# Kernel tuning notes

Hardware: AMD Instinct MI355X
Metric: run time of the kernel (lower is better)

Reference implementation:

```python
import jax, jax.numpy as jnp
import numpy as np

BATCH, T, D_MODEL, DIM = 8, 4096, 512, 512
R_MIN, R_MAX, MAX_PHASE = 0.0, 1.0, 6.28


def setup_inputs() -> dict:
    key = jax.random.key(0)
    ks = jax.random.split(key, 8)
    x = jax.random.normal(ks[0], (BATCH, T, D_MODEL), dtype=jnp.float32)
    h0 = jnp.zeros((BATCH, 1, DIM), dtype=jnp.float32)
    # nu_log / theta_log per the module's initializers
    u1 = jax.random.uniform(ks[1], (DIM,))
    nu_log = jnp.log(-0.5 * jnp.log(u1 * (R_MAX ** 2 - R_MIN ** 2) + R_MIN ** 2)).astype(jnp.float32)
    u2 = jax.random.uniform(ks[2], (DIM,))
    theta_log = jnp.log(MAX_PHASE * u2).astype(jnp.float32)
    # B ~ N(0,1)/sqrt(2*D_in), C ~ N(0,1)/sqrt(D_out)
    B_re = (jax.random.normal(ks[3], (D_MODEL, DIM)) / jnp.sqrt(2.0 * D_MODEL)).astype(jnp.float32)
    B_im = (jax.random.normal(ks[4], (D_MODEL, DIM)) / jnp.sqrt(2.0 * D_MODEL)).astype(jnp.float32)
    C_re = (jax.random.normal(ks[5], (DIM, D_MODEL)) / jnp.sqrt(float(D_MODEL))).astype(jnp.float32)
    C_im = (jax.random.normal(ks[6], (DIM, D_MODEL)) / jnp.sqrt(float(D_MODEL))).astype(jnp.float32)
    D_param = jax.random.normal(ks[7], (D_MODEL,)).astype(jnp.float32)
    # gamma_log = log(sqrt(1 - |Lambda|^2)) with Lambda from nu/theta
    diag_lambda = jnp.exp(-jnp.exp(nu_log) + 1j * jnp.exp(theta_log))
    gamma_log = jnp.log(jnp.sqrt(1.0 - jnp.abs(diag_lambda) ** 2)).astype(jnp.float32)
    return {"x": x, "h0": h0, "nu_log": nu_log, "theta_log": theta_log,
            "B_re": B_re, "B_im": B_im, "C_re": C_re, "C_im": C_im,
            "D_param": D_param, "gamma_log": gamma_log}


def _binary_op(ei, ej):
    a_i, b_i = ei
    a_j, b_j = ej
    return (a_j * a_i, a_j * b_i + b_j)


def reference(x, h0, nu_log, theta_log, B_re, B_im, C_re, C_im, D_param, gamma_log):
    B, T_len, _ = x.shape
    Lambda = jnp.exp(-jnp.exp(nu_log) + 1j * jnp.exp(theta_log))            # (N,) complex
    B_norm = (B_re + 1j * B_im) * jnp.exp(gamma_log)[None, :]               # (D,N) complex
    C = C_re + 1j * C_im                                                     # (N,D) complex
    # Input projection: Bu[b,t,n] = sum_d x[b,t,d] * B_norm[d,n]
    Bu = jnp.einsum('btd,dn->btn', x.astype(jnp.complex64), B_norm)
    Bu = jnp.concatenate([h0.astype(jnp.complex64), Bu], axis=1)             # (B,T+1,N)
    Lam = jnp.broadcast_to(Lambda, Bu.shape)                                 # (B,T+1,N)
    _, H = jax.lax.associative_scan(_binary_op, (Lam, Bu), axis=1)
    H = H[:, 1:]                                                             # (B,T,N)
    y = jnp.einsum('btn,nd->btd', H, C).real + D_param * x                   # (B,T,D)
    new_h = H[:, -1:]                                                        # (B,1,N) complex
    return (y, new_h)
```

## Files before the change

kernel.cpp:

```cpp
#include <hip/hip_runtime.h>

#define T_LEN 4096
#define DMODEL 512
#define DIM 512
#define NBATCH 8
#define MROWS (NBATCH * T_LEN)
#define NCHUNK 128
#define LCHUNK 32

typedef __attribute__((ext_vector_type(8))) short short8;
typedef __attribute__((ext_vector_type(4))) float float4v;

__device__ __forceinline__ ushort f2b(float f) {
    union { float fl; unsigned u; } v; v.fl = f;
    unsigned u = v.u;
    return (ushort)((u + 0x7FFFu + ((u >> 16) & 1u)) >> 16);
}
__device__ __forceinline__ float b2f(ushort u) {
    union { unsigned u; float f; } v; v.u = (unsigned)u << 16; return v.f;
}

__device__ __forceinline__ void glds16(const ushort* g, ushort* l) {
    __builtin_amdgcn_global_load_lds(
        (const __attribute__((address_space(1))) void*)g,
        (__attribute__((address_space(3))) void*)l, 16, 0, 0);
}

#define XBLK (MROWS * 512 / 4 / 256)
#define BBLK (1024 * 512 / 256)
#define CBLK (512 * 1024 / 256)

__global__ __launch_bounds__(256) void k_prep(const float* __restrict__ x,
                                              const float* __restrict__ B_re,
                                              const float* __restrict__ B_im,
                                              const float* __restrict__ gamma_log,
                                              const float* __restrict__ C_re,
                                              const float* __restrict__ C_im,
                                              ushort* __restrict__ Xb,
                                              ushort* __restrict__ BT,
                                              ushort* __restrict__ CT) {
    int bb = blockIdx.x;
    if (bb < XBLK) {
        int i = (bb * 256 + threadIdx.x) * 4;
        float4 v = *(const float4*)(x + i);
        ushort4 o;
        o.x = f2b(v.x); o.y = f2b(v.y); o.z = f2b(v.z); o.w = f2b(v.w);
        *(ushort4*)(Xb + i) = o;
    } else if (bb < XBLK + BBLK) {
        int idx = (bb - XBLK) * 256 + threadIdx.x;
        int n = idx >> 9;
        int d = idx & 511;
        float v;
        if (n < 512) v = B_re[d * 512 + n] * __expf(gamma_log[n]);
        else { int nn = n - 512; v = B_im[d * 512 + nn] * __expf(gamma_log[nn]); }
        BT[idx] = f2b(v);
    } else {
        int idx = (bb - XBLK - BBLK) * 256 + threadIdx.x;
        int d = idx >> 10;
        int k = idx & 1023;
        float v = (k < 512) ? C_re[k * 512 + d] : -C_im[(k - 512) * 512 + d];
        CT[idx] = f2b(v);
    }
}


template<int K>
__device__ __forceinline__ void stage_tile(const ushort* gA0, const ushort* gB0, int kt,
                                           ushort* sAb, ushort* sBb, int wave) {
#pragma unroll
    for (int c = 0; c < 4; c++) {
        glds16(gA0 + (size_t)(c * 8) * K + (size_t)kt * 64, &sAb[(wave * 32 + c * 8) * 64]);
        glds16(gB0 + (size_t)(c * 8) * K + (size_t)kt * 64, &sBb[(wave * 32 + c * 8) * 64]);
    }
}

__device__ __forceinline__ void compute_tile(const ushort* sAb, const ushort* sBb,
                                             int wm, int wn, int lr, int quad,
                                             float4v acc[4][4]) {
#pragma unroll
    for (int kk = 0; kk < 2; kk++) {
        short8 af[4], bfr[4];
#pragma unroll
        for (int i = 0; i < 4; i++) {
            int row = wm + i * 16 + lr;
            af[i] = *(const short8*)&sAb[row * 64 + (((kk * 4 + quad) ^ (row & 7)) * 8)];
        }
#pragma unroll
        for (int j = 0; j < 4; j++) {
            int row = wn + j * 16 + lr;
            bfr[j] = *(const short8*)&sBb[row * 64 + (((kk * 4 + quad) ^ (row & 7)) * 8)];
        }
#pragma unroll
        for (int i = 0; i < 4; i++)
#pragma unroll
            for (int j = 0; j < 4; j++)
                acc[i][j] = __builtin_amdgcn_mfma_f32_16x16x32_bf16(af[i], bfr[j], acc[i][j], 0, 0, 0);
    }
}

template<int K, int MODE, int NBN>
__global__ __launch_bounds__(256) void k_gemm(
    const ushort* __restrict__ A, const ushort* __restrict__ Bt,
    ushort* __restrict__ oRe, ushort* __restrict__ oIm,
    float* __restrict__ y, const float* __restrict__ x, const float* __restrict__ Dp) {
    __shared__ ushort sA[2][128 * 64];
    __shared__ ushort sB[2][128 * 64];
    const int tid = threadIdx.x;
    const int L = blockIdx.x;
    const int xcd = L & 7;
    const int slot = L >> 3;
    const int m0 = (xcd * 32 + slot / NBN) * 128;
    const int n0 = (slot % NBN) * 128;
    const int wave = tid >> 6;
    const int lane = tid & 63;
    const int wm = (wave >> 1) * 64;
    const int wn = (wave & 1) * 64;
    const int lr = lane & 15;
    const int quad = lane >> 4;

    const int srow = lane >> 3;
    const int schunk = (lane & 7) ^ srow;
    const ushort* gA0 = A + (size_t)(m0 + wave * 32 + srow) * K + schunk * 8;
    const ushort* gB0 = Bt + (size_t)(n0 + wave * 32 + srow) * K + schunk * 8;

    float4v acc[4][4];
#pragma unroll
    for (int i = 0; i < 4; i++)
#pragma unroll
        for (int j = 0; j < 4; j++) {
            float4v z = {0.f, 0.f, 0.f, 0.f};
            acc[i][j] = z;
        }

    const int NT = K / 64;

    stage_tile<K>(gA0, gB0, 0, &sA[0][0], &sB[0][0], wave);
    __syncthreads();

    for (int t = 0; t < NT; t += 2) {
        stage_tile<K>(gA0, gB0, t + 1, &sA[1][0], &sB[1][0], wave);
        compute_tile(&sA[0][0], &sB[0][0], wm, wn, lr, quad, acc);
        __syncthreads();

        if (t + 2 < NT)
            stage_tile<K>(gA0, gB0, t + 2, &sA[0][0], &sB[0][0], wave);
        compute_tile(&sA[1][0], &sB[1][0], wm, wn, lr, quad, acc);
        __syncthreads();
    }

#pragma unroll
    for (int i = 0; i < 4; i++) {
#pragma unroll
        for (int j = 0; j < 4; j++) {
            int gmb = m0 + wm + i * 16 + quad * 4;
            int gn = n0 + wn + j * 16 + lr;
#pragma unroll
            for (int r = 0; r < 4; r++) {
                float v = acc[i][j][r];
                int row = gmb + r;
                if (MODE == 1) {
                    if (gn < 512) oRe[(size_t)row * 512 + gn] = f2b(v);
                    else oIm[(size_t)row * 512 + (gn - 512)] = f2b(v);
                } else {
                    size_t o = (size_t)row * 512 + gn;
                    y[o] = v + Dp[gn] * x[o];
                }
            }
        }
    }
}


__device__ __forceinline__ void lambda_of(const float* nu_log, const float* theta_log,
                                          int n, float& lre, float& lim) {
    float e = __expf(nu_log[n]);
    float th = __expf(theta_log[n]);
    float rad = __expf(-e);
    float s, c;
    __sincosf(th, &s, &c);
    lre = rad * c;
    lim = rad * s;
}

__global__ __launch_bounds__(256) void k_scan1(const ushort* __restrict__ BuRe,
                                               const ushort* __restrict__ BuIm,
                                               const float* __restrict__ nu_log,
                                               const float* __restrict__ theta_log,
                                               float* __restrict__ cRe, float* __restrict__ cIm) {
    int n2 = threadIdx.x;
    int b = blockIdx.x >> 7;
    int c = blockIdx.x & 127;
    float lre0, lim0, lre1, lim1;
    lambda_of(nu_log, theta_log, 2 * n2, lre0, lim0);
    lambda_of(nu_log, theta_log, 2 * n2 + 1, lre1, lim1);
    float hr0 = 0.f, hi0 = 0.f, hr1 = 0.f, hi1 = 0.f;
    size_t base = ((size_t)b * T_LEN + (size_t)c * LCHUNK) * 512 + 2 * n2;
#pragma unroll 8
    for (int j = 0; j < LCHUNK; j++) {
        ushort2 ur = *(const ushort2*)(BuRe + base + (size_t)j * 512);
        ushort2 ui = *(const ushort2*)(BuIm + base + (size_t)j * 512);
        float br0 = b2f(ur.x), br1 = b2f(ur.y), bi0 = b2f(ui.x), bi1 = b2f(ui.y);
        float nr0 = lre0 * hr0 - lim0 * hi0 + br0;
        float ni0 = lre0 * hi0 + lim0 * hr0 + bi0;
        hr0 = nr0; hi0 = ni0;
        float nr1 = lre1 * hr1 - lim1 * hi1 + br1;
        float ni1 = lre1 * hi1 + lim1 * hr1 + bi1;
        hr1 = nr1; hi1 = ni1;
    }
    size_t co = ((size_t)b * NCHUNK + c) * 512 + 2 * n2;
    *(float2*)(cRe + co) = make_float2(hr0, hr1);
    *(float2*)(cIm + co) = make_float2(hi0, hi1);
}

__global__ __launch_bounds__(64) void k_scan2(const float* __restrict__ cRe,
                                              const float* __restrict__ cIm,
                                              const float* __restrict__ h0,
                                              const float* __restrict__ nu_log,
                                              const float* __restrict__ theta_log,
                                              float* __restrict__ pRe, float* __restrict__ pIm,
                                              float* __restrict__ newH, int newh_mode) {
    int idx = blockIdx.x * 64 + threadIdx.x;
    int b = idx >> 9;
    int n = idx & 511;
    float lre, lim;
    lambda_of(nu_log, theta_log, n, lre, lim);
    float Lr = lre, Li = lim;
#pragma unroll
    for (int s = 0; s < 5; s++) {
        float nr = Lr * Lr - Li * Li;
        float ni = 2.f * Lr * Li;
        Lr = nr; Li = ni;
    }
    float cr = h0[b * 512 + n];
    float ci = 0.f;
#pragma unroll 4
    for (int c = 0; c < NCHUNK; c++) {
        size_t o = ((size_t)b * NCHUNK + c) * 512 + n;
        pRe[o] = cr;
        pIm[o] = ci;
        float ar = cRe[o], ai = cIm[o];
        float nr = Lr * cr - Li * ci + ar;
        float ni = Lr * ci + Li * cr + ai;
        cr = nr; ci = ni;
    }
    size_t ci_idx = (size_t)b * 512 + n;
    if (newh_mode == 1) {
        newH[ci_idx] = cr;
        newH[(size_t)NBATCH * 512 + ci_idx] = ci;
    } else if (newh_mode == 2) {
        newH[ci_idx] = cr;
    } else {
        newH[ci_idx * 2] = cr;
        newH[ci_idx * 2 + 1] = ci;
    }
}

__global__ __launch_bounds__(256) void k_scan3(const ushort* __restrict__ BuRe,
                                               const ushort* __restrict__ BuIm,
                                               const float* __restrict__ pRe,
                                               const float* __restrict__ pIm,
                                               const float* __restrict__ nu_log,
                                               const float* __restrict__ theta_log,
                                               ushort* __restrict__ Hbf) {
    int n2 = threadIdx.x;
    int b = blockIdx.x >> 7;
    int c = blockIdx.x & 127;
    float lre0, lim0, lre1, lim1;
    lambda_of(nu_log, theta_log, 2 * n2, lre0, lim0);
    lambda_of(nu_log, theta_log, 2 * n2 + 1, lre1, lim1);
    size_t co = ((size_t)b * NCHUNK + c) * 512 + 2 * n2;
    float2 frv = *(const float2*)(pRe + co);
    float2 fiv = *(const float2*)(pIm + co);
    float fr0 = frv.x, fr1 = frv.y, fi0 = fiv.x, fi1 = fiv.y;
    float pr0 = lre0, pi0 = lim0, pr1 = lre1, pi1 = lim1;
    float hr0 = 0.f, hi0 = 0.f, hr1 = 0.f, hi1 = 0.f;
    size_t row0 = (size_t)b * T_LEN + (size_t)c * LCHUNK;
#pragma unroll 4
    for (int j = 0; j < LCHUNK; j++) {
        size_t base = (row0 + j) * 512 + 2 * n2;
        ushort2 ur = *(const ushort2*)(BuRe + base);
        ushort2 ui = *(const ushort2*)(BuIm + base);
        float br0 = b2f(ur.x), br1 = b2f(ur.y), bi0 = b2f(ui.x), bi1 = b2f(ui.y);
        float nr0 = lre0 * hr0 - lim0 * hi0 + br0;
        float ni0 = lre0 * hi0 + lim0 * hr0 + bi0;
        hr0 = nr0; hi0 = ni0;
        float nr1 = lre1 * hr1 - lim1 * hi1 + br1;
        float ni1 = lre1 * hi1 + lim1 * hr1 + bi1;
        hr1 = nr1; hi1 = ni1;
        float vr0 = hr0 + pr0 * fr0 - pi0 * fi0;
        float vi0 = hi0 + pr0 * fi0 + pi0 * fr0;
        float vr1 = hr1 + pr1 * fr1 - pi1 * fi1;
        float vi1 = hi1 + pr1 * fi1 + pi1 * fr1;
        size_t hrow = (row0 + j) * 1024;
        ushort2 wre, wim;
        wre.x = f2b(vr0); wre.y = f2b(vr1);
        wim.x = f2b(vi0); wim.y = f2b(vi1);
        *(ushort2*)(Hbf + hrow + 2 * n2) = wre;
        *(ushort2*)(Hbf + hrow + 512 + 2 * n2) = wim;
        float npr0 = pr0 * lre0 - pi0 * lim0;
        float npi0 = pr0 * lim0 + pi0 * lre0;
        pr0 = npr0; pi0 = npi0;
        float npr1 = pr1 * lre1 - pi1 * lim1;
        float npi1 = pr1 * lim1 + pi1 * lre1;
        pr1 = npr1; pi1 = npi1;
    }
}


extern "C" void kernel_launch(void* const* d_in, const int* in_sizes, int n_in,
                              void* d_out, int out_size, void* d_ws, size_t ws_size,
                              hipStream_t stream) {
    const float* x         = (const float*)d_in[0];
    const float* h0        = (const float*)d_in[1];
    const float* nu_log    = (const float*)d_in[2];
    const float* theta_log = (const float*)d_in[3];
    const float* B_re      = (const float*)d_in[4];
    const float* B_im      = (const float*)d_in[5];
    const float* C_re      = (const float*)d_in[6];
    const float* C_im      = (const float*)d_in[7];
    const float* D_param   = (const float*)d_in[8];
    const float* gamma_log = (const float*)d_in[9];

    char* ws = (char*)d_ws;
    size_t off = 0;
    ushort* Xb   = (ushort*)(ws + off); off += (size_t)MROWS * 512 * 2;
    ushort* BT   = (ushort*)(ws + off); off += (size_t)1024 * 512 * 2;
    ushort* CT   = (ushort*)(ws + off); off += (size_t)512 * 1024 * 2;
    ushort* BuRe = (ushort*)(ws + off); off += (size_t)MROWS * 512 * 2;
    ushort* BuIm = (ushort*)(ws + off); off += (size_t)MROWS * 512 * 2;
    ushort* Hbf  = (ushort*)(ws + off); off += (size_t)MROWS * 1024 * 2;
    float*  cRe  = (float*)(ws + off); off += (size_t)NBATCH * NCHUNK * 512 * 4;
    float*  cIm  = (float*)(ws + off); off += (size_t)NBATCH * NCHUNK * 512 * 4;
    float*  pRe  = (float*)(ws + off); off += (size_t)NBATCH * NCHUNK * 512 * 4;
    float*  pIm  = (float*)(ws + off); off += (size_t)NBATCH * NCHUNK * 512 * 4;

    float* y_out = (float*)d_out;
    float* newH  = (float*)d_out + (size_t)MROWS * 512;

    const int tail = out_size - MROWS * 512;
    int newh_mode = 0;
    if (tail == NBATCH * 512 * 2) newh_mode = 1;
    else if (tail == NBATCH * 512) newh_mode = 2;

    k_prep<<<dim3(XBLK + BBLK + CBLK), dim3(256), 0, stream>>>(
        x, B_re, B_im, gamma_log, C_re, C_im, Xb, BT, CT);

    k_gemm<512, 1, 8><<<dim3(2048), dim3(256), 0, stream>>>(
        Xb, BT, BuRe, BuIm, nullptr, nullptr, nullptr);

    k_scan1<<<dim3(NBATCH * NCHUNK), dim3(256), 0, stream>>>(BuRe, BuIm, nu_log, theta_log, cRe, cIm);
    k_scan2<<<dim3(NBATCH * 512 / 64), dim3(64), 0, stream>>>(cRe, cIm, h0, nu_log, theta_log, pRe, pIm, newH, newh_mode);
    k_scan3<<<dim3(NBATCH * NCHUNK), dim3(256), 0, stream>>>(BuRe, BuIm, pRe, pIm, nu_log, theta_log, Hbf);

    k_gemm<1024, 2, 4><<<dim3(1024), dim3(256), 0, stream>>>(
        Hbf, CT, nullptr, nullptr, y_out, x, D_param);
}
```

Before: 287.2 us.

## Enlarge GEMM tiles to 256x128 with 8 waves and triple-buffered LDS pipeline

Both bf16 MFMA GEMMs now use 256x128 block tiles with 512 threads instead of 128x128 with 256. The old double-buffered loop with __syncthreads is replaced by a triple-buffered ring: tiles are prefetched two steps ahead and each step waits with explicit vmcnt counts and raw s_barrier calls. MFMA sections are wrapped in s_setprio. The aim is to hide global-to-LDS load latency and improve operand reuse. In exchange, LDS use grows to about 144KB per block, which leaves one block per CU and halves the grid size. An unused helper that passes a null LDS pointer is also added.

```diff
diff --git a/kernel.cpp b/kernel.cpp
--- a/kernel.cpp
+++ b/kernel.cpp
@@ -64,14 +64,23 @@
 }
 
 
+__device__ __forceinline__ void stage_tileA(const ushort* gA0, long koff, ushort* sAb,
+                                            int wave) {
+#pragma unroll
+    for (int c = 0; c < 4; c++)
+        glds16(gA0 + (long)(c * 8) * 0 + koff + 0, nullptr);
+}
+
 template<int K>
 __device__ __forceinline__ void stage_tile(const ushort* gA0, const ushort* gB0, int kt,
                                            ushort* sAb, ushort* sBb, int wave) {
-#pragma unroll
-    for (int c = 0; c < 4; c++) {
-        glds16(gA0 + (size_t)(c * 8) * K + (size_t)kt * 64, &sAb[(wave * 32 + c * 8) * 64]);
-        glds16(gB0 + (size_t)(c * 8) * K + (size_t)kt * 64, &sBb[(wave * 32 + c * 8) * 64]);
-    }
+    const long ko = (long)kt * 64;
+#pragma unroll
+    for (int c = 0; c < 4; c++)
+        glds16(gA0 + (long)(c * 8) * K + ko, &sAb[(wave * 32 + c * 8) * 64]);
+#pragma unroll
+    for (int c = 0; c < 2; c++)
+        glds16(gB0 + (long)(c * 8) * K + ko, &sBb[(wave * 16 + c * 8) * 64]);
 }
 
 __device__ __forceinline__ void compute_tile(const ushort* sAb, const ushort* sBb,
@@ -90,26 +99,29 @@
             int row = wn + j * 16 + lr;
             bfr[j] = *(const short8*)&sBb[row * 64 + (((kk * 4 + quad) ^ (row & 7)) * 8)];
         }
+        __builtin_amdgcn_s_setprio(1);
 #pragma unroll
         for (int i = 0; i < 4; i++)
 #pragma unroll
             for (int j = 0; j < 4; j++)
                 acc[i][j] = __builtin_amdgcn_mfma_f32_16x16x32_bf16(af[i], bfr[j], acc[i][j], 0, 0, 0);
+        __builtin_amdgcn_s_setprio(0);
     }
 }
 
 template<int K, int MODE, int NBN>
-__global__ __launch_bounds__(256) void k_gemm(
+__global__ __launch_bounds__(512) void k_gemm(
     const ushort* __restrict__ A, const ushort* __restrict__ Bt,
     ushort* __restrict__ oRe, ushort* __restrict__ oIm,
     float* __restrict__ y, const float* __restrict__ x, const float* __restrict__ Dp) {
-    __shared__ ushort sA[2][128 * 64];
-    __shared__ ushort sB[2][128 * 64];
+    const int NT = K / 64;
+    __shared__ ushort sA[3][256 * 64];
+    __shared__ ushort sB[3][128 * 64];
     const int tid = threadIdx.x;
     const int L = blockIdx.x;
     const int xcd = L & 7;
     const int slot = L >> 3;
-    const int m0 = (xcd * 32 + slot / NBN) * 128;
+    const int m0 = (xcd * 16 + slot / NBN) * 256;
     const int n0 = (slot % NBN) * 128;
     const int wave = tid >> 6;
     const int lane = tid & 63;
@@ -121,7 +133,7 @@
     const int srow = lane >> 3;
     const int schunk = (lane & 7) ^ srow;
     const ushort* gA0 = A + (size_t)(m0 + wave * 32 + srow) * K + schunk * 8;
-    const ushort* gB0 = Bt + (size_t)(n0 + wave * 32 + srow) * K + schunk * 8;
+    const ushort* gB0 = Bt + (size_t)(n0 + wave * 16 + srow) * K + schunk * 8;
 
     float4v acc[4][4];
 #pragma unroll
@@ -132,20 +144,28 @@
             acc[i][j] = z;
         }
 
-    const int NT = K / 64;
-
-    stage_tile<K>(gA0, gB0, 0, &sA[0][0], &sB[0][0], wave);
-    __syncthreads();
-
-    for (int t = 0; t < NT; t += 2) {
-        stage_tile<K>(gA0, gB0, t + 1, &sA[1][0], &sB[1][0], wave);
-        compute_tile(&sA[0][0], &sB[0][0], wm, wn, lr, quad, acc);
-        __syncthreads();
-
+    ushort *a0 = &sA[0][0], *a1 = &sA[1][0], *a2 = &sA[2][0];
+    ushort *b0 = &sB[0][0], *b1 = &sB[1][0], *b2 = &sB[2][0];
+
+    stage_tile<K>(gA0, gB0, 0, a0, b0, wave);
+    stage_tile<K>(gA0, gB0, 1, a1, b1, wave);
+    asm volatile("s_waitcnt vmcnt(6)" ::: "memory");
+    __builtin_amdgcn_s_barrier();
+    __builtin_amdgcn_sched_barrier(0);
+
+    for (int t = 0; t < NT; ++t) {
         if (t + 2 < NT)
-            stage_tile<K>(gA0, gB0, t + 2, &sA[0][0], &sB[0][0], wave);
-        compute_tile(&sA[1][0], &sB[1][0], wm, wn, lr, quad, acc);
-        __syncthreads();
+            stage_tile<K>(gA0, gB0, t + 2, a2, b2, wave);
+        compute_tile(a0, b0, wm, wn, lr, quad, acc);
+        if (t + 2 < NT) {
+            asm volatile("s_waitcnt vmcnt(6)" ::: "memory");
+        } else {
+            asm volatile("s_waitcnt vmcnt(0)" ::: "memory");
+        }
+        __builtin_amdgcn_s_barrier();
+        __builtin_amdgcn_sched_barrier(0);
+        ushort* ta = a0; a0 = a1; a1 = a2; a2 = ta;
+        ushort* tb = b0; b0 = b1; b1 = b2; b2 = tb;
     }
 
 #pragma unroll
@@ -345,13 +365,13 @@
     k_prep<<<dim3(XBLK + BBLK + CBLK), dim3(256), 0, stream>>>(
         x, B_re, B_im, gamma_log, C_re, C_im, Xb, BT, CT);
 
-    k_gemm<512, 1, 8><<<dim3(2048), dim3(256), 0, stream>>>(
+    k_gemm<512, 1, 8><<<dim3(1024), dim3(512), 0, stream>>>(
         Xb, BT, BuRe, BuIm, nullptr, nullptr, nullptr);
 
     k_scan1<<<dim3(NBATCH * NCHUNK), dim3(256), 0, stream>>>(BuRe, BuIm, nu_log, theta_log, cRe, cIm);
     k_scan2<<<dim3(NBATCH * 512 / 64), dim3(64), 0, stream>>>(cRe, cIm, h0, nu_log, theta_log, pRe, pIm, newH, newh_mode);
     k_scan3<<<dim3(NBATCH * NCHUNK), dim3(256), 0, stream>>>(BuRe, BuIm, pRe, pIm, nu_log, theta_log, Hbf);
 
-    k_gemm<1024, 2, 4><<<dim3(1024), dim3(256), 0, stream>>>(
+    k_gemm<1024, 2, 4><<<dim3(512), dim3(512), 0, stream>>>(
         Hbf, CT, nullptr, nullptr, y_out, x, D_param);
 }
```

Result: slower. 305.3 us (+6.3%).
